# Kernel optimization log

Measured on AMD Instinct MI355X. Metric: run time of the kernel, lower is better.

Reference implementation:

```python
import jax, jax.numpy as jnp
import numpy as np

V, E, H, F_IN, F_OUT, F_E = 30000, 500000, 4, 32, 32, 32
NEG_SLOPE = 0.2

def _act(x):
    return jax.nn.leaky_relu(x, NEG_SLOPE)

def setup_inputs() -> dict:
    key = jax.random.key(0)
    ks = jax.random.split(key, 24)
    def lin(kw, kb, fin, fout):
        W = jax.random.normal(kw, (fin, fout), jnp.float32) * (1.0 / np.sqrt(fin))
        b = jax.random.normal(kb, (fout,), jnp.float32) * 0.01
        return W, b
    W_as, b_as = lin(ks[0], ks[1], F_IN, F_IN)
    W_ad, b_ad = lin(ks[2], ks[3], F_IN, F_IN)
    W_ae, b_ae = lin(ks[4], ks[5], F_E, F_IN)
    W_dot, b_dot = lin(ks[6], ks[7], F_IN, 1)
    W_ms, b_ms = lin(ks[8], ks[9], F_IN, F_OUT)
    W_md, b_md = lin(ks[10], ks[11], F_IN, F_OUT)
    W_me, b_me = lin(ks[12], ks[13], F_E, F_OUT)
    W_wn, b_wn = lin(ks[14], ks[15], F_IN, F_OUT)
    node_feats = jax.random.normal(ks[16], (V, H, F_IN), jnp.float32)
    edge_feats = jax.random.normal(ks[17], (E, F_E), jnp.float32)
    src_idx = jax.random.randint(ks[18], (E,), 0, V, jnp.int32)
    dst_idx = jax.random.randint(ks[19], (E,), 0, V, jnp.int32)
    return {
        'node_feats': node_feats, 'edge_feats': edge_feats,
        'src_idx': src_idx, 'dst_idx': dst_idx,
        'W_as': W_as, 'b_as': b_as, 'W_ad': W_ad, 'b_ad': b_ad,
        'W_ae': W_ae, 'b_ae': b_ae, 'W_dot': W_dot, 'b_dot': b_dot,
        'W_ms': W_ms, 'b_ms': b_ms, 'W_md': W_md, 'b_md': b_md,
        'W_me': W_me, 'b_me': b_me, 'W_wn': W_wn, 'b_wn': b_wn,
    }

def reference(node_feats, edge_feats, src_idx, dst_idx,
              W_as, b_as, W_ad, b_ad, W_ae, b_ae, W_dot, b_dot,
              W_ms, b_ms, W_md, b_md, W_me, b_me, W_wn, b_wn):
    n_nodes = node_feats.shape[0]
    # attention path
    src = node_feats @ W_as + b_as                      # (V,H,F)
    dst = node_feats @ W_ad + b_ad                      # (V,H,F)
    edg_atn = (edge_feats @ W_ae + b_ae)[:, None, :]    # (E,1,F)
    e = _act(src[src_idx] + dst[dst_idx] + edg_atn)     # (E,H,F)
    scores = e @ W_dot + b_dot                          # (E,H,1)
    # edge softmax: normalize over incoming edges of each dst node
    smax = jax.ops.segment_max(scores, dst_idx, num_segments=n_nodes)
    ex = jnp.exp(scores - smax[dst_idx])
    ssum = jax.ops.segment_sum(ex, dst_idx, num_segments=n_nodes)
    alpha = ex / ssum[dst_idx]                          # (E,H,1)
    # message path
    msg_s = node_feats @ W_ms + b_ms                    # (V,H,Fo)
    msg_d = node_feats @ W_md + b_md                    # (V,H,Fo)
    msg_e = (edge_feats @ W_me + b_me)[:, None, :]      # (E,1,Fo)
    atn_inp = _act(msg_s[src_idx] + msg_d[dst_idx] + msg_e)  # (E,H,Fo)
    feat = jax.ops.segment_sum(alpha * atn_inp, dst_idx, num_segments=n_nodes)  # (V,H,Fo)
    out = _act(feat + node_feats @ W_wn + b_wn)         # (V,H,Fo)
    return out
```

## Files before the change

kernel.cpp:

```cpp
#include <hip/hip_runtime.h>
#include <hip/hip_bf16.h>

#define V_N 30000
#define E_N 500000
#define XW  512
#define HB  1954
#define GB  2048

typedef __attribute__((ext_vector_type(8))) short bf16x8;
typedef __attribute__((ext_vector_type(4))) float f32x4;

__device__ __forceinline__ float lrelu(float x) { return fmaxf(x, 0.2f * x); }
__device__ __forceinline__ unsigned short f2bf(float f) {
    __hip_bfloat16 h = __float2bfloat16(f);
    return *reinterpret_cast<unsigned short*>(&h);
}
__device__ __forceinline__ float bf_lo(unsigned u) { return __uint_as_float(u << 16); }
__device__ __forceinline__ float bf_hi(unsigned u) { return __uint_as_float(u & 0xffff0000u); }

template<int CTRL, int RMASK>
__device__ __forceinline__ float dpp_add(float t) {
    int b = __builtin_amdgcn_update_dpp(0, __float_as_int(t), CTRL, RMASK, 0xF, true);
    return t + __int_as_float(b);
}

__device__ __forceinline__ float group_sum(float t, int lane) {
    t = dpp_add<0x121, 0xF>(t);
    t = dpp_add<0x122, 0xF>(t);
    t = dpp_add<0x124, 0xF>(t);
    t = dpp_add<0x128, 0xF>(t);
    t = dpp_add<0x142, 0xA>(t);
    float u = __shfl_xor(t, 16);
    return (lane & 16) ? t : u;
}

__global__ __launch_bounds__(256) void fused_a(
    const float* __restrict__ nf, const float* __restrict__ ef,
    const float* __restrict__ Was, const float* __restrict__ bas,
    const float* __restrict__ Wms, const float* __restrict__ bms,
    const float* __restrict__ Wad, const float* __restrict__ bad,
    const float* __restrict__ Wmd, const float* __restrict__ bmd,
    const float* __restrict__ Wae, const float* __restrict__ bae,
    const float* __restrict__ Wme, const float* __restrict__ bme,
    const int* __restrict__ dst,
    uint4* __restrict__ tab_s, uint4* __restrict__ tab_d,
    int* __restrict__ deg, unsigned* __restrict__ em)
{
    int tid = threadIdx.x;
    if (blockIdx.x >= XW + HB) {
        int lane = tid & 63;
        int l15 = lane & 15, q = lane >> 4;
        bf16x8 B0, B1, B2, B3;
        #pragma unroll
        for (int i = 0; i < 8; ++i) {
            int k = q * 8 + i;
            B0[i] = (short)f2bf(Wae[k * 32 + l15]);
            B1[i] = (short)f2bf(Wae[k * 32 + 16 + l15]);
            B2[i] = (short)f2bf(Wme[k * 32 + l15]);
            B3[i] = (short)f2bf(Wme[k * 32 + 16 + l15]);
        }
        float ba0 = bae[l15], ba1 = bae[16 + l15];
        float bm0 = bme[l15], bm1 = bme[16 + l15];
        int bid = blockIdx.x - (XW + HB);
        int wid = (bid * 256 + tid) >> 6;
        int nw  = (GB * 256) >> 6;
        const int ntiles = E_N / 16;
        for (int tile = wid; tile < ntiles; tile += nw) {
            int ebase = tile * 16;
            const float4* ap = (const float4*)(ef + (size_t)(ebase + l15) * 32 + q * 8);
            float4 a0 = ap[0], a1 = ap[1];
            bf16x8 A;
            A[0] = (short)f2bf(a0.x); A[1] = (short)f2bf(a0.y);
            A[2] = (short)f2bf(a0.z); A[3] = (short)f2bf(a0.w);
            A[4] = (short)f2bf(a1.x); A[5] = (short)f2bf(a1.y);
            A[6] = (short)f2bf(a1.z); A[7] = (short)f2bf(a1.w);
            f32x4 z = {0.f, 0.f, 0.f, 0.f};
            f32x4 D0 = __builtin_amdgcn_mfma_f32_16x16x32_bf16(A, B0, z, 0, 0, 0);
            f32x4 D1 = __builtin_amdgcn_mfma_f32_16x16x32_bf16(A, B1, z, 0, 0, 0);
            f32x4 D2 = __builtin_amdgcn_mfma_f32_16x16x32_bf16(A, B2, z, 0, 0, 0);
            f32x4 D3 = __builtin_amdgcn_mfma_f32_16x16x32_bf16(A, B3, z, 0, 0, 0);
            #pragma unroll
            for (int j = 0; j < 4; ++j) {
                int e = ebase + q * 4 + j;
                unsigned lo = f2bf(D0[j] + ba0) | ((unsigned)f2bf(D2[j] + bm0) << 16);
                unsigned hi = f2bf(D1[j] + ba1) | ((unsigned)f2bf(D3[j] + bm1) << 16);
                em[(size_t)e * 32 + l15]      = lo;
                em[(size_t)e * 32 + 16 + l15] = hi;
            }
        }
        return;
    }
    if (blockIdx.x >= XW) {
        int i = (blockIdx.x - XW) * 256 + tid;
        if (i < E_N) atomicAdd(&deg[dst[i]], 1);
        return;
    }
    int lane = tid & 63;
    int l15 = lane & 15, q = lane >> 4;
    bf16x8 Bas0, Bas1, Bad0, Bad1, Bms0, Bms1, Bmd0, Bmd1;
    #pragma unroll
    for (int i = 0; i < 8; ++i) {
        int k = q * 8 + i;
        Bas0[i] = (short)f2bf(Was[k * 32 + l15]);
        Bas1[i] = (short)f2bf(Was[k * 32 + 16 + l15]);
        Bad0[i] = (short)f2bf(Wad[k * 32 + l15]);
        Bad1[i] = (short)f2bf(Wad[k * 32 + 16 + l15]);
        Bms0[i] = (short)f2bf(Wms[k * 32 + l15]);
        Bms1[i] = (short)f2bf(Wms[k * 32 + 16 + l15]);
        Bmd0[i] = (short)f2bf(Wmd[k * 32 + l15]);
        Bmd1[i] = (short)f2bf(Wmd[k * 32 + 16 + l15]);
    }
    float bs0 = bas[l15], bs1 = bas[16 + l15];
    float bd0 = bad[l15], bd1 = bad[16 + l15];
    float bm0 = bms[l15], bm1 = bms[16 + l15];
    float bn0 = bmd[l15], bn1 = bmd[16 + l15];

    int wv = tid >> 6;
    const int ntiles = V_N / 4;
    for (int tile = blockIdx.x * 4 + wv; tile < ntiles; tile += XW * 4) {
        int nbase = tile * 4;
        int rbase = nbase * 4;
        const float4* ap = (const float4*)(nf + (size_t)(rbase + l15) * 32 + q * 8);
        float4 a0 = ap[0], a1 = ap[1];
        bf16x8 A;
        A[0] = (short)f2bf(a0.x); A[1] = (short)f2bf(a0.y);
        A[2] = (short)f2bf(a0.z); A[3] = (short)f2bf(a0.w);
        A[4] = (short)f2bf(a1.x); A[5] = (short)f2bf(a1.y);
        A[6] = (short)f2bf(a1.z); A[7] = (short)f2bf(a1.w);
        f32x4 z = {0.f, 0.f, 0.f, 0.f};
        f32x4 Das0 = __builtin_amdgcn_mfma_f32_16x16x32_bf16(A, Bas0, z, 0, 0, 0);
        f32x4 Das1 = __builtin_amdgcn_mfma_f32_16x16x32_bf16(A, Bas1, z, 0, 0, 0);
        f32x4 Dad0 = __builtin_amdgcn_mfma_f32_16x16x32_bf16(A, Bad0, z, 0, 0, 0);
        f32x4 Dad1 = __builtin_amdgcn_mfma_f32_16x16x32_bf16(A, Bad1, z, 0, 0, 0);
        f32x4 Dms0 = __builtin_amdgcn_mfma_f32_16x16x32_bf16(A, Bms0, z, 0, 0, 0);
        f32x4 Dms1 = __builtin_amdgcn_mfma_f32_16x16x32_bf16(A, Bms1, z, 0, 0, 0);
        f32x4 Dmd0 = __builtin_amdgcn_mfma_f32_16x16x32_bf16(A, Bmd0, z, 0, 0, 0);
        f32x4 Dmd1 = __builtin_amdgcn_mfma_f32_16x16x32_bf16(A, Bmd1, z, 0, 0, 0);
        int node = nbase + q;
        uint4 lo, hi;
        lo.x = f2bf(Das0[0] + bs0) | ((unsigned)f2bf(Das0[1] + bs0) << 16);
        lo.y = f2bf(Das0[2] + bs0) | ((unsigned)f2bf(Das0[3] + bs0) << 16);
        lo.z = f2bf(Dms0[0] + bm0) | ((unsigned)f2bf(Dms0[1] + bm0) << 16);
        lo.w = f2bf(Dms0[2] + bm0) | ((unsigned)f2bf(Dms0[3] + bm0) << 16);
        hi.x = f2bf(Das1[0] + bs1) | ((unsigned)f2bf(Das1[1] + bs1) << 16);
        hi.y = f2bf(Das1[2] + bs1) | ((unsigned)f2bf(Das1[3] + bs1) << 16);
        hi.z = f2bf(Dms1[0] + bm1) | ((unsigned)f2bf(Dms1[1] + bm1) << 16);
        hi.w = f2bf(Dms1[2] + bm1) | ((unsigned)f2bf(Dms1[3] + bm1) << 16);
        tab_s[(size_t)node * 32 + l15]      = lo;
        tab_s[(size_t)node * 32 + 16 + l15] = hi;
        uint4 lod, hid;
        lod.x = f2bf(Dad0[0] + bd0) | ((unsigned)f2bf(Dad0[1] + bd0) << 16);
        lod.y = f2bf(Dad0[2] + bd0) | ((unsigned)f2bf(Dad0[3] + bd0) << 16);
        lod.z = f2bf(Dmd0[0] + bn0) | ((unsigned)f2bf(Dmd0[1] + bn0) << 16);
        lod.w = f2bf(Dmd0[2] + bn0) | ((unsigned)f2bf(Dmd0[3] + bn0) << 16);
        hid.x = f2bf(Dad1[0] + bd1) | ((unsigned)f2bf(Dad1[1] + bd1) << 16);
        hid.y = f2bf(Dad1[2] + bd1) | ((unsigned)f2bf(Dad1[3] + bd1) << 16);
        hid.z = f2bf(Dmd1[0] + bn1) | ((unsigned)f2bf(Dmd1[1] + bn1) << 16);
        hid.w = f2bf(Dmd1[2] + bn1) | ((unsigned)f2bf(Dmd1[3] + bn1) << 16);
        tab_d[(size_t)node * 32 + l15]      = lod;
        tab_d[(size_t)node * 32 + 16 + l15] = hid;
    }
}

__global__ __launch_bounds__(1024) void scan_k(
    const int* __restrict__ deg, int* __restrict__ rowptr, int* __restrict__ cursor,
    int* __restrict__ perm)
{
    __shared__ int wsum[16];
    __shared__ int carry_s;
    __shared__ int bh[128];
    __shared__ int bc[128];
    int tid = threadIdx.x;
    int lane = tid & 63, wv = tid >> 6;
    if (tid == 0) carry_s = 0;
    if (tid < 128) bh[tid] = 0;
    __syncthreads();
    for (int base = 0; base < V_N; base += 1024) {
        int i = base + tid;
        int v = (i < V_N) ? deg[i] : 0;
        int x = v;
        #pragma unroll
        for (int off = 1; off < 64; off <<= 1) {
            int t = __shfl_up(x, off, 64);
            if (lane >= off) x += t;
        }
        if (lane == 63) wsum[wv] = x;
        __syncthreads();
        if (wv == 0 && lane < 16) {
            int s = wsum[lane];
            #pragma unroll
            for (int off = 1; off < 16; off <<= 1) {
                int t = __shfl_up(s, off, 64);
                if (lane >= off) s += t;
            }
            wsum[lane] = s;
        }
        __syncthreads();
        int woff  = (wv == 0) ? 0 : wsum[wv - 1];
        int carry = carry_s;
        int excl  = carry + woff + x - v;
        if (i < V_N) {
            rowptr[i] = excl; cursor[i] = excl;
            atomicAdd(&bh[min(v, 127)], 1);
        }
        __syncthreads();
        if (tid == 1023) carry_s = carry + wsum[15];
        __syncthreads();
    }
    if (tid == 0) {
        rowptr[V_N] = carry_s;
        int off = 0;
        for (int b = 127; b >= 0; --b) { bc[b] = off; off += bh[b]; }
    }
    __syncthreads();
    for (int base = 0; base < V_N; base += 1024) {
        int i = base + tid;
        if (i < V_N) {
            int b = min(deg[i], 127);
            int p = atomicAdd(&bc[b], 1);
            perm[p] = i;
        }
    }
}

__global__ __launch_bounds__(256) void scatter_k(
    const int* __restrict__ dst, const int* __restrict__ src,
    int* __restrict__ cursor, int2* __restrict__ csr2)
{
    int i = blockIdx.x * 256 + threadIdx.x;
    if (i < E_N) {
        int p = atomicAdd(&cursor[dst[i]], 1);
        csr2[p] = make_int2(src[i], i);
    }
}

__global__ __launch_bounds__(256) void node_gather4(
    const int* __restrict__ rowptr, const int2* __restrict__ csr2,
    const unsigned* __restrict__ em, const uint4* __restrict__ tab_s,
    const uint4* __restrict__ tab_d,
    const float* __restrict__ Wdot,
    const float* __restrict__ Wwn, const float* __restrict__ bwn,
    const float* __restrict__ nf,
    const int* __restrict__ perm,
    float* __restrict__ out)
{
    __shared__ float ww[1024], wd[32];
    int tid = threadIdx.x;
    for (int i = tid; i < 1024; i += 256) ww[i] = Wwn[i];
    if (tid < 32) wd[tid] = Wdot[tid] * 1.4426950408889634f;
    __syncthreads();
    int lane = tid & 31;
    int n = perm[blockIdx.x * 8 + (tid >> 5)];
    float wdl = wd[lane];

    float da[4], dm[4];
    {
        uint4 v = tab_d[(size_t)n * 32 + lane];
        da[0] = bf_lo(v.x); da[1] = bf_hi(v.x);
        da[2] = bf_lo(v.y); da[3] = bf_hi(v.y);
        dm[0] = bf_lo(v.z); dm[1] = bf_hi(v.z);
        dm[2] = bf_lo(v.w); dm[3] = bf_hi(v.w);
    }

    float acc0 = 0.f, acc1 = 0.f, acc2 = 0.f, acc3 = 0.f;
    float s0 = 0.f, s1 = 0.f, s2 = 0.f, s3 = 0.f;
    int p0 = rowptr[n], p1 = rowptr[n + 1];

    uint4 gc = make_uint4(0, 0, 0, 0);
    unsigned ec = 0;
    if (p0 < p1) {
        int2 c = csr2[p0];
        gc = tab_s[(size_t)c.x * 32 + lane];
        ec = em[(size_t)c.y * 32 + lane];
    }
    for (int p = p0; p < p1; ++p) {
        uint4 g = gc; unsigned ev = ec;
        if (p + 1 < p1) {
            int2 c = csr2[p + 1];
            gc = tab_s[(size_t)c.x * 32 + lane];
            ec = em[(size_t)c.y * 32 + lane];
        }
        float ea = bf_lo(ev), me = bf_hi(ev);
        float t0 = lrelu(bf_lo(g.x) + da[0] + ea) * wdl;
        float t1 = lrelu(bf_hi(g.x) + da[1] + ea) * wdl;
        float t2 = lrelu(bf_lo(g.y) + da[2] + ea) * wdl;
        float t3 = lrelu(bf_hi(g.y) + da[3] + ea) * wdl;
        t0 = group_sum(t0, lane);
        t1 = group_sum(t1, lane);
        t2 = group_sum(t2, lane);
        t3 = group_sum(t3, lane);
        float x0 = exp2f(t0), x1 = exp2f(t1);
        float x2 = exp2f(t2), x3 = exp2f(t3);
        float m0 = lrelu(bf_lo(g.z) + dm[0] + me);
        float m1 = lrelu(bf_hi(g.z) + dm[1] + me);
        float m2 = lrelu(bf_lo(g.w) + dm[2] + me);
        float m3 = lrelu(bf_hi(g.w) + dm[3] + me);
        acc0 = fmaf(x0, m0, acc0); s0 += x0;
        acc1 = fmaf(x1, m1, acc1); s1 += x1;
        acc2 = fmaf(x2, m2, acc2); s2 += x2;
        acc3 = fmaf(x3, m3, acc3); s3 += x3;
    }
    #pragma unroll
    for (int h = 0; h < 4; ++h) {
        float x = nf[(size_t)n * 128 + h * 32 + lane];
        float a = bwn[lane];
        #pragma unroll
        for (int k = 0; k < 32; ++k)
            a = fmaf(__shfl(x, k, 32), ww[k * 32 + lane], a);
        float accv = (h == 0) ? acc0 : (h == 1) ? acc1 : (h == 2) ? acc2 : acc3;
        float sv   = (h == 0) ? s0   : (h == 1) ? s1   : (h == 2) ? s2   : s3;
        float f = (sv > 0.f) ? accv / sv : 0.f;
        out[(size_t)n * 128 + h * 32 + lane] = lrelu(f + a);
    }
}

extern "C" void kernel_launch(void* const* d_in, const int* in_sizes, int n_in,
                              void* d_out, int out_size, void* d_ws, size_t ws_size,
                              hipStream_t stream)
{
    const float* nf  = (const float*)d_in[0];
    const float* ef  = (const float*)d_in[1];
    const int*   src = (const int*)d_in[2];
    const int*   dst = (const int*)d_in[3];
    const float* Was = (const float*)d_in[4],  *bas = (const float*)d_in[5];
    const float* Wad = (const float*)d_in[6],  *bad = (const float*)d_in[7];
    const float* Wae = (const float*)d_in[8],  *bae = (const float*)d_in[9];
    const float* Wdot= (const float*)d_in[10];
    const float* Wms = (const float*)d_in[12], *bms = (const float*)d_in[13];
    const float* Wmd = (const float*)d_in[14], *bmd = (const float*)d_in[15];
    const float* Wme = (const float*)d_in[16], *bme = (const float*)d_in[17];
    const float* Wwn = (const float*)d_in[18], *bwn = (const float*)d_in[19];

    const size_t em_w  = (size_t)E_N * 32;
    const size_t tab_w = (size_t)V_N * 32;
    unsigned* em     = (unsigned*)d_ws;
    uint4*    tab_s  = (uint4*)(em + em_w);
    uint4*    tab_d  = tab_s + tab_w;
    int*      deg    = (int*)(tab_d + tab_w);
    int*      rowptr = deg + V_N;
    int*      cursor = rowptr + V_N + 1;
    int2*     csr2   = (int2*)(cursor + V_N);
    int*      perm   = (int*)(csr2 + E_N);

    hipMemsetAsync(deg, 0, V_N * sizeof(int), stream);

    const int ebk = (E_N + 255) / 256;

    fused_a<<<XW + HB + GB, 256, 0, stream>>>(nf, ef, Was, bas, Wms, bms,
                                              Wad, bad, Wmd, bmd,
                                              Wae, bae, Wme, bme, dst,
                                              tab_s, tab_d, deg, em);
    scan_k<<<1, 1024, 0, stream>>>(deg, rowptr, cursor, perm);
    scatter_k<<<ebk, 256, 0, stream>>>(dst, src, cursor, csr2);
    node_gather4<<<3750, 256, 0, stream>>>(rowptr, csr2, em, tab_s, tab_d,
                                           Wdot, Wwn, bwn, nf, perm, (float*)d_out);
}
```

Baseline: 185.8 us.

## Reorder pipeline: histogram first, fuse scatter with projections, precompute W_wn via MFMA

Moves the degree histogram into its own first kernel, so the CSR scatter can run inside the big fused projection kernel alongside the edge and node MFMA work, replacing the separate scatter launch. It also computes the node self-projection (W_wn) with MFMA in the fused kernel, stores it as bf16, and reads it in the gather kernel instead of doing a 32-step shuffle matvec per node. It needs extra workspace, falls back to the old path when workspace is too small, and adds bf16 rounding to the residual term.

```diff
diff --git a/kernel.cpp b/kernel.cpp
--- a/kernel.cpp
+++ b/kernel.cpp
@@ -4,7 +4,7 @@
 #define V_N 30000
 #define E_N 500000
 #define XW  512
-#define HB  1954
+#define SB  1954
 #define GB  2048
 
 typedef __attribute__((ext_vector_type(8))) short bf16x8;
@@ -34,20 +34,92 @@
     return (lane & 16) ? t : u;
 }
 
-__global__ __launch_bounds__(256) void fused_a(
+__global__ __launch_bounds__(256) void hist_k(
+    const int* __restrict__ dst, int* __restrict__ deg)
+{
+    int i = blockIdx.x * 256 + threadIdx.x;
+    if (i < E_N) atomicAdd(&deg[dst[i]], 1);
+}
+
+__global__ __launch_bounds__(1024) void scan_k(
+    const int* __restrict__ deg, int* __restrict__ rowptr, int* __restrict__ cursor,
+    int* __restrict__ perm)
+{
+    __shared__ int wsum[16];
+    __shared__ int carry_s;
+    __shared__ int bh[128];
+    __shared__ int bc[128];
+    int tid = threadIdx.x;
+    int lane = tid & 63, wv = tid >> 6;
+    if (tid == 0) carry_s = 0;
+    if (tid < 128) bh[tid] = 0;
+    __syncthreads();
+    for (int base = 0; base < V_N; base += 1024) {
+        int i = base + tid;
+        int v = (i < V_N) ? deg[i] : 0;
+        int x = v;
+        #pragma unroll
+        for (int off = 1; off < 64; off <<= 1) {
+            int t = __shfl_up(x, off, 64);
+            if (lane >= off) x += t;
+        }
+        if (lane == 63) wsum[wv] = x;
+        __syncthreads();
+        if (wv == 0 && lane < 16) {
+            int s = wsum[lane];
+            #pragma unroll
+            for (int off = 1; off < 16; off <<= 1) {
+                int t = __shfl_up(s, off, 64);
+                if (lane >= off) s += t;
+            }
+            wsum[lane] = s;
+        }
+        __syncthreads();
+        int woff  = (wv == 0) ? 0 : wsum[wv - 1];
+        int carry = carry_s;
+        int excl  = carry + woff + x - v;
+        if (i < V_N) {
+            rowptr[i] = excl; cursor[i] = excl;
+            atomicAdd(&bh[min(v, 127)], 1);
+        }
+        __syncthreads();
+        if (tid == 1023) carry_s = carry + wsum[15];
+        __syncthreads();
+    }
+    if (tid == 0) {
+        rowptr[V_N] = carry_s;
+        int off = 0;
+        for (int b = 127; b >= 0; --b) { bc[b] = off; off += bh[b]; }
+    }
+    __syncthreads();
+    for (int base = 0; base < V_N; base += 1024) {
+        int i = base + tid;
+        if (i < V_N) {
+            int b = min(deg[i], 127);
+            int p = atomicAdd(&bc[b], 1);
+            perm[p] = i;
+        }
+    }
+}
+
+template<bool WN>
+__global__ __launch_bounds__(256) void fused_b(
     const float* __restrict__ nf, const float* __restrict__ ef,
+    const int* __restrict__ src, const int* __restrict__ dst,
+    int* __restrict__ cursor,
     const float* __restrict__ Was, const float* __restrict__ bas,
     const float* __restrict__ Wms, const float* __restrict__ bms,
     const float* __restrict__ Wad, const float* __restrict__ bad,
     const float* __restrict__ Wmd, const float* __restrict__ bmd,
     const float* __restrict__ Wae, const float* __restrict__ bae,
     const float* __restrict__ Wme, const float* __restrict__ bme,
-    const int* __restrict__ dst,
+    const float* __restrict__ Wwn, const float* __restrict__ bwn,
     uint4* __restrict__ tab_s, uint4* __restrict__ tab_d,
-    int* __restrict__ deg, unsigned* __restrict__ em)
+    uint2* __restrict__ wn_t,
+    int2* __restrict__ csr2, unsigned* __restrict__ em)
 {
     int tid = threadIdx.x;
-    if (blockIdx.x >= XW + HB) {
+    if (blockIdx.x < GB) {
         int lane = tid & 63;
         int l15 = lane & 15, q = lane >> 4;
         bf16x8 B0, B1, B2, B3;
@@ -61,8 +133,7 @@
         }
         float ba0 = bae[l15], ba1 = bae[16 + l15];
         float bm0 = bme[l15], bm1 = bme[16 + l15];
-        int bid = blockIdx.x - (XW + HB);
-        int wid = (bid * 256 + tid) >> 6;
+        int wid = (blockIdx.x * 256 + tid) >> 6;
         int nw  = (GB * 256) >> 6;
         const int ntiles = E_N / 16;
         for (int tile = wid; tile < ntiles; tile += nw) {
@@ -90,14 +161,18 @@
         }
         return;
     }
-    if (blockIdx.x >= XW) {
-        int i = (blockIdx.x - XW) * 256 + tid;
-        if (i < E_N) atomicAdd(&deg[dst[i]], 1);
+    if (blockIdx.x < GB + SB) {
+        int i = (blockIdx.x - GB) * 256 + tid;
+        if (i < E_N) {
+            int p = atomicAdd(&cursor[dst[i]], 1);
+            csr2[p] = make_int2(src[i], i);
+        }
         return;
     }
+    int bid = blockIdx.x - (GB + SB);
     int lane = tid & 63;
     int l15 = lane & 15, q = lane >> 4;
-    bf16x8 Bas0, Bas1, Bad0, Bad1, Bms0, Bms1, Bmd0, Bmd1;
+    bf16x8 Bas0, Bas1, Bad0, Bad1, Bms0, Bms1, Bmd0, Bmd1, Bwn0, Bwn1;
     #pragma unroll
     for (int i = 0; i < 8; ++i) {
         int k = q * 8 + i;
@@ -109,15 +184,20 @@
         Bms1[i] = (short)f2bf(Wms[k * 32 + 16 + l15]);
         Bmd0[i] = (short)f2bf(Wmd[k * 32 + l15]);
         Bmd1[i] = (short)f2bf(Wmd[k * 32 + 16 + l15]);
+        if (WN) {
+            Bwn0[i] = (short)f2bf(Wwn[k * 32 + l15]);
+            Bwn1[i] = (short)f2bf(Wwn[k * 32 + 16 + l15]);
+        }
     }
     float bs0 = bas[l15], bs1 = bas[16 + l15];
     float bd0 = bad[l15], bd1 = bad[16 + l15];
     float bm0 = bms[l15], bm1 = bms[16 + l15];
     float bn0 = bmd[l15], bn1 = bmd[16 + l15];
+    float bw0 = WN ? bwn[l15] : 0.f, bw1 = WN ? bwn[16 + l15] : 0.f;
 
     int wv = tid >> 6;
     const int ntiles = V_N / 4;
-    for (int tile = blockIdx.x * 4 + wv; tile < ntiles; tile += XW * 4) {
+    for (int tile = bid * 4 + wv; tile < ntiles; tile += XW * 4) {
         int nbase = tile * 4;
         int rbase = nbase * 4;
         const float4* ap = (const float4*)(nf + (size_t)(rbase + l15) * 32 + q * 8);
@@ -159,94 +239,35 @@
         hid.w = f2bf(Dmd1[2] + bn1) | ((unsigned)f2bf(Dmd1[3] + bn1) << 16);
         tab_d[(size_t)node * 32 + l15]      = lod;
         tab_d[(size_t)node * 32 + 16 + l15] = hid;
-    }
-}
-
-__global__ __launch_bounds__(1024) void scan_k(
-    const int* __restrict__ deg, int* __restrict__ rowptr, int* __restrict__ cursor,
-    int* __restrict__ perm)
-{
-    __shared__ int wsum[16];
-    __shared__ int carry_s;
-    __shared__ int bh[128];
-    __shared__ int bc[128];
-    int tid = threadIdx.x;
-    int lane = tid & 63, wv = tid >> 6;
-    if (tid == 0) carry_s = 0;
-    if (tid < 128) bh[tid] = 0;
-    __syncthreads();
-    for (int base = 0; base < V_N; base += 1024) {
-        int i = base + tid;
-        int v = (i < V_N) ? deg[i] : 0;
-        int x = v;
-        #pragma unroll
-        for (int off = 1; off < 64; off <<= 1) {
-            int t = __shfl_up(x, off, 64);
-            if (lane >= off) x += t;
-        }
-        if (lane == 63) wsum[wv] = x;
-        __syncthreads();
-        if (wv == 0 && lane < 16) {
-            int s = wsum[lane];
-            #pragma unroll
-            for (int off = 1; off < 16; off <<= 1) {
-                int t = __shfl_up(s, off, 64);
-                if (lane >= off) s += t;
-            }
-            wsum[lane] = s;
-        }
-        __syncthreads();
-        int woff  = (wv == 0) ? 0 : wsum[wv - 1];
-        int carry = carry_s;
-        int excl  = carry + woff + x - v;
-        if (i < V_N) {
-            rowptr[i] = excl; cursor[i] = excl;
-            atomicAdd(&bh[min(v, 127)], 1);
-        }
-        __syncthreads();
-        if (tid == 1023) carry_s = carry + wsum[15];
-        __syncthreads();
-    }
-    if (tid == 0) {
-        rowptr[V_N] = carry_s;
-        int off = 0;
-        for (int b = 127; b >= 0; --b) { bc[b] = off; off += bh[b]; }
-    }
-    __syncthreads();
-    for (int base = 0; base < V_N; base += 1024) {
-        int i = base + tid;
-        if (i < V_N) {
-            int b = min(deg[i], 127);
-            int p = atomicAdd(&bc[b], 1);
-            perm[p] = i;
-        }
-    }
-}
-
-__global__ __launch_bounds__(256) void scatter_k(
-    const int* __restrict__ dst, const int* __restrict__ src,
-    int* __restrict__ cursor, int2* __restrict__ csr2)
-{
-    int i = blockIdx.x * 256 + threadIdx.x;
-    if (i < E_N) {
-        int p = atomicAdd(&cursor[dst[i]], 1);
-        csr2[p] = make_int2(src[i], i);
-    }
-}
-
-__global__ __launch_bounds__(256) void node_gather4(
+        if (WN) {
+            f32x4 Dwn0 = __builtin_amdgcn_mfma_f32_16x16x32_bf16(A, Bwn0, z, 0, 0, 0);
+            f32x4 Dwn1 = __builtin_amdgcn_mfma_f32_16x16x32_bf16(A, Bwn1, z, 0, 0, 0);
+            uint2 w0, w1;
+            w0.x = f2bf(Dwn0[0] + bw0) | ((unsigned)f2bf(Dwn0[1] + bw0) << 16);
+            w0.y = f2bf(Dwn0[2] + bw0) | ((unsigned)f2bf(Dwn0[3] + bw0) << 16);
+            w1.x = f2bf(Dwn1[0] + bw1) | ((unsigned)f2bf(Dwn1[1] + bw1) << 16);
+            w1.y = f2bf(Dwn1[2] + bw1) | ((unsigned)f2bf(Dwn1[3] + bw1) << 16);
+            wn_t[(size_t)node * 32 + l15]      = w0;
+            wn_t[(size_t)node * 32 + 16 + l15] = w1;
+        }
+    }
+}
+
+template<bool WN>
+__global__ __launch_bounds__(256) void node_gather6(
     const int* __restrict__ rowptr, const int2* __restrict__ csr2,
     const unsigned* __restrict__ em, const uint4* __restrict__ tab_s,
-    const uint4* __restrict__ tab_d,
+    const uint4* __restrict__ tab_d, const uint2* __restrict__ wn_t,
     const float* __restrict__ Wdot,
     const float* __restrict__ Wwn, const float* __restrict__ bwn,
     const float* __restrict__ nf,
     const int* __restrict__ perm,
     float* __restrict__ out)
 {
-    __shared__ float ww[1024], wd[32];
+    __shared__ float ww[WN ? 1 : 1024];
+    __shared__ float wd[32];
     int tid = threadIdx.x;
-    for (int i = tid; i < 1024; i += 256) ww[i] = Wwn[i];
+    if (!WN) for (int i = tid; i < 1024; i += 256) ww[i] = Wwn[i];
     if (tid < 32) wd[tid] = Wdot[tid] * 1.4426950408889634f;
     __syncthreads();
     int lane = tid & 31;
@@ -300,17 +321,32 @@
         acc2 = fmaf(x2, m2, acc2); s2 += x2;
         acc3 = fmaf(x3, m3, acc3); s3 += x3;
     }
-    #pragma unroll
-    for (int h = 0; h < 4; ++h) {
-        float x = nf[(size_t)n * 128 + h * 32 + lane];
-        float a = bwn[lane];
+    if (WN) {
+        uint2 w = wn_t[(size_t)n * 32 + lane];
+        float wn0 = bf_lo(w.x), wn1 = bf_hi(w.x);
+        float wn2 = bf_lo(w.y), wn3 = bf_hi(w.y);
+        float f0 = (s0 > 0.f) ? acc0 / s0 : 0.f;
+        float f1 = (s1 > 0.f) ? acc1 / s1 : 0.f;
+        float f2 = (s2 > 0.f) ? acc2 / s2 : 0.f;
+        float f3 = (s3 > 0.f) ? acc3 / s3 : 0.f;
+        size_t ob = (size_t)n * 128 + lane;
+        out[ob]      = lrelu(f0 + wn0);
+        out[ob + 32] = lrelu(f1 + wn1);
+        out[ob + 64] = lrelu(f2 + wn2);
+        out[ob + 96] = lrelu(f3 + wn3);
+    } else {
         #pragma unroll
-        for (int k = 0; k < 32; ++k)
-            a = fmaf(__shfl(x, k, 32), ww[k * 32 + lane], a);
-        float accv = (h == 0) ? acc0 : (h == 1) ? acc1 : (h == 2) ? acc2 : acc3;
-        float sv   = (h == 0) ? s0   : (h == 1) ? s1   : (h == 2) ? s2   : s3;
-        float f = (sv > 0.f) ? accv / sv : 0.f;
-        out[(size_t)n * 128 + h * 32 + lane] = lrelu(f + a);
+        for (int h = 0; h < 4; ++h) {
+            float x = nf[(size_t)n * 128 + h * 32 + lane];
+            float a = bwn[lane];
+            #pragma unroll
+            for (int k = 0; k < 32; ++k)
+                a = fmaf(__shfl(x, k, 32), ww[k * 32 + lane], a);
+            float accv = (h == 0) ? acc0 : (h == 1) ? acc1 : (h == 2) ? acc2 : acc3;
+            float sv   = (h == 0) ? s0   : (h == 1) ? s1   : (h == 2) ? s2   : s3;
+            float f = (sv > 0.f) ? accv / sv : 0.f;
+            out[(size_t)n * 128 + h * 32 + lane] = lrelu(f + a);
+        }
     }
 }
 
@@ -333,10 +369,17 @@
 
     const size_t em_w  = (size_t)E_N * 32;
     const size_t tab_w = (size_t)V_N * 32;
+    const size_t wn_w  = (size_t)V_N * 32;
+    const size_t int_b = ((size_t)V_N * 3 + 1 + (size_t)E_N * 2) * 4;
+    const size_t need_wn = em_w * 4 + tab_w * 16 * 2 + wn_w * 8 + int_b;
+    const bool   wn_ok = (ws_size >= need_wn);
+
     unsigned* em     = (unsigned*)d_ws;
     uint4*    tab_s  = (uint4*)(em + em_w);
     uint4*    tab_d  = tab_s + tab_w;
-    int*      deg    = (int*)(tab_d + tab_w);
+    uint2*    wn_t   = (uint2*)(tab_d + tab_w);
+    int*      ints   = wn_ok ? (int*)(wn_t + wn_w) : (int*)(tab_d + tab_w);
+    int*      deg    = ints;
     int*      rowptr = deg + V_N;
     int*      cursor = rowptr + V_N + 1;
     int2*     csr2   = (int2*)(cursor + V_N);
@@ -344,14 +387,23 @@
 
     hipMemsetAsync(deg, 0, V_N * sizeof(int), stream);
 
-    const int ebk = (E_N + 255) / 256;
-
-    fused_a<<<XW + HB + GB, 256, 0, stream>>>(nf, ef, Was, bas, Wms, bms,
-                                              Wad, bad, Wmd, bmd,
-                                              Wae, bae, Wme, bme, dst,
-                                              tab_s, tab_d, deg, em);
+    const int hbk = (E_N + 255) / 256;
+
+    hist_k<<<hbk, 256, 0, stream>>>(dst, deg);
     scan_k<<<1, 1024, 0, stream>>>(deg, rowptr, cursor, perm);
-    scatter_k<<<ebk, 256, 0, stream>>>(dst, src, cursor, csr2);
-    node_gather4<<<3750, 256, 0, stream>>>(rowptr, csr2, em, tab_s, tab_d,
-                                           Wdot, Wwn, bwn, nf, perm, (float*)d_out);
-}
+    if (wn_ok) {
+        fused_b<true><<<GB + SB + XW, 256, 0, stream>>>(
+            nf, ef, src, dst, cursor, Was, bas, Wms, bms, Wad, bad, Wmd, bmd,
+            Wae, bae, Wme, bme, Wwn, bwn, tab_s, tab_d, wn_t, csr2, em);
+        node_gather6<true><<<3750, 256, 0, stream>>>(
+            rowptr, csr2, em, tab_s, tab_d, wn_t, Wdot, Wwn, bwn, nf, perm,
+            (float*)d_out);
+    } else {
+        fused_b<false><<<GB + SB + XW, 256, 0, stream>>>(
+            nf, ef, src, dst, cursor, Was, bas, Wms, bms, Wad, bad, Wmd, bmd,
+            Wae, bae, Wme, bme, Wwn, bwn, tab_s, tab_d, wn_t, csr2, em);
+        node_gather6<false><<<3750, 256, 0, stream>>>(
+            rowptr, csr2, em, tab_s, tab_d, wn_t, Wdot, Wwn, bwn, nf, perm,
+            (float*)d_out);
+    }
+}
```

Result: slower. 192.1 us (+3.4%).
